# Kernel tuning notes

Hardware: AMD Instinct MI355X
Metric: run time of the kernel (lower is better)

## Reference

```python
import jax, jax.numpy as jnp
import numpy as np

D_MODEL = 1024
N_HEADS = 16


def setup_inputs() -> dict:
    key = jax.random.key(0)
    ks = jax.random.split(key, 5)
    B, T, C = 4, 2048, D_MODEL
    x = jax.random.normal(ks[0], (B, T, C), dtype=jnp.float32)
    W_attn = jax.random.normal(ks[1], (C, 3 * C), dtype=jnp.float32) * (1.0 / np.sqrt(C))
    b_attn = jnp.zeros((3 * C,), dtype=jnp.float32)
    W_proj = jax.random.normal(ks[2], (C, C), dtype=jnp.float32) * (1.0 / np.sqrt(C))
    b_proj = jnp.zeros((C,), dtype=jnp.float32)
    return {"x": x, "W_attn": W_attn, "b_attn": b_attn, "W_proj": W_proj, "b_proj": b_proj}


def reference(x, W_attn, b_attn, W_proj, b_proj):
    B, T, C = x.shape
    H = N_HEADS
    hd = C // H
    qkv = x @ W_attn + b_attn                      # [B,T,3C]
    q, k, v = jnp.split(qkv, 3, axis=2)
    # [B,T,C] -> [B,H,T,hd]
    q = q.reshape(B, T, H, hd).transpose(0, 2, 1, 3)
    k = k.reshape(B, T, H, hd).transpose(0, 2, 1, 3)
    v = v.reshape(B, T, H, hd).transpose(0, 2, 1, 3)
    scale = 1.0 / jnp.sqrt(jnp.float32(hd))
    attn = jnp.einsum('bhqd,bhkd->bhqk', q, k) * scale
    causal = jnp.tril(jnp.ones((T, T), dtype=bool))
    attn = jnp.where(causal[None, None], attn, -jnp.inf)
    w = jax.nn.softmax(attn, axis=-1)
    ctx = jnp.einsum('bhqk,bhkd->bhqd', w, v)      # [B,H,T,hd]
    ctx = ctx.transpose(0, 2, 1, 3).reshape(B, T, C)
    return ctx @ W_proj + b_proj
```

## Files before the change

kernel.cpp:

```cpp
#include <hip/hip_runtime.h>
#include <hip/hip_bf16.h>

typedef __bf16 bf16x8 __attribute__((ext_vector_type(8)));
typedef __bf16 bf16x4 __attribute__((ext_vector_type(4)));
typedef float f32x4 __attribute__((ext_vector_type(4)));

#define MFMA(A, B, C) __builtin_amdgcn_mfma_f32_16x16x32_bf16((A), (B), (C), 0, 0, 0)

#if __has_builtin(__builtin_amdgcn_exp2f)
#define EXP2(x) __builtin_amdgcn_exp2f(x)
#else
#define EXP2(x) exp2f(x)
#endif

#define T_SEQ 2048
#define BATCH 4
#define CDIM  1024
#define HEADS 16
#define HD    64
#define MROWS (BATCH * T_SEQ)
#define QK_SCALE 0.18033688011112042f
#define KTILES (CDIM / 64)

__device__ __forceinline__ void async_ld16(const __bf16* g, __bf16* l) {
    __builtin_amdgcn_global_load_lds(
        (const __attribute__((address_space(1))) void*)g,
        (__attribute__((address_space(3))) void*)l, 16, 0, 0);
}

__global__ __launch_bounds__(256) void conv_transpose(const float* __restrict__ src,
                                                      __bf16* __restrict__ dst,
                                                      int R, int C)
{
    __shared__ float tile[32][33];
    int c0 = blockIdx.x * 32, r0 = blockIdx.y * 32;
    int tx = threadIdx.x, ty = threadIdx.y;
#pragma unroll
    for (int i = 0; i < 4; i++)
        tile[ty + i * 8][tx] = src[(long)(r0 + ty + i * 8) * C + c0 + tx];
    __syncthreads();
#pragma unroll
    for (int i = 0; i < 4; i++)
        dst[(long)(c0 + ty + i * 8) * R + r0 + tx] = (__bf16)tile[tx][ty + i * 8];
}

__global__ __launch_bounds__(256) void conv_bf16(const float* __restrict__ src,
                                                 __bf16* __restrict__ dst)
{
    long i = ((long)blockIdx.x * 256 + threadIdx.x) * 8;
    f32x4 f0 = ((const f32x4*)(src + i))[0];
    f32x4 f1 = ((const f32x4*)(src + i))[1];
    bf16x8 v;
#pragma unroll
    for (int j = 0; j < 4; j++) { v[j] = (__bf16)f0[j]; v[4 + j] = (__bf16)f1[j]; }
    *(bf16x8*)(dst + i) = v;
}

__global__ __launch_bounds__(256) void vtrans(const __bf16* __restrict__ qkv,
                                              __bf16* __restrict__ vt)
{
    __shared__ __bf16 tile[32][33];
    int bh = blockIdx.z;
    int b = bh >> 4, h = bh & 15;
    int t0 = blockIdx.x * 32, d0 = blockIdx.y * 32;
    int tx = threadIdx.x, ty = threadIdx.y;
#pragma unroll
    for (int i = 0; i < 4; i++)
        tile[ty + i * 8][tx] =
            qkv[(long)(b * T_SEQ + t0 + ty + i * 8) * (3 * CDIM) + 2 * CDIM + h * HD + d0 + tx];
    __syncthreads();
#pragma unroll
    for (int i = 0; i < 4; i++)
        vt[(long)(bh * HD + d0 + ty + i * 8) * T_SEQ + t0 + tx] = tile[tx][ty + i * 8];
}

#define STAGE_A(buf, kt, s)                                                      \
    do {                                                                         \
        async_ld16(Asrc + (long)((s) * 64) * lda + (kt) * 64,                    \
                   &lds[buf][0][(s) * 4096 + sdst]);                             \
        async_ld16(Asrc + (long)((s) * 64 + 128) * lda + (kt) * 64,              \
                   &lds[buf][0][(s) * 4096 + 8192 + sdst]);                      \
    } while (0)

#define STAGE_B(buf, kt, s)                                                      \
    do {                                                                         \
        async_ld16(Bsrc + (long)((s) * 128) * CDIM + (kt) * 64,                  \
                   &lds[buf][1][(s) * 8192 + sdst]);                             \
        async_ld16(Bsrc + (long)((s) * 128 + 64) * CDIM + (kt) * 64,             \
                   &lds[buf][1][(s) * 8192 + 4096 + sdst]);                      \
    } while (0)

template <bool OUT_F32>
__global__ __launch_bounds__(512, 2) void gemm8p(const __bf16* __restrict__ A,
                                                 const __bf16* __restrict__ Bt,
                                                 const float* __restrict__ bias,
                                                 void* __restrict__ Cv,
                                                 int N, int lda, int scale_cols)
{
    __shared__ __attribute__((aligned(16))) __bf16 lds[2][2][256 * 64];

    const int nwg = (int)gridDim.x;
    const int bid = (int)blockIdx.x;
    const int swz = (bid & 7) * (nwg >> 3) + (bid >> 3);
    const int nbx = N >> 8;
    const int n0 = (swz % nbx) * 256;
    const int m0 = (swz / nbx) * 256;

    const int t = threadIdx.x;
    const int wave = t >> 6, lane = t & 63;
    const int quad = lane >> 4, l15 = lane & 15;
    const int wm = wave >> 2;
    const int wn = wave & 3;

    const int srow = t >> 3;
    const int scol = ((t & 7) * 8) ^ ((srow & 7) << 3);
    const int sdst = srow * 64 + (t & 7) * 8;
    const __bf16* Asrc = A + (long)(m0 + srow) * lda + scol;
    const __bf16* Bsrc = Bt + (long)(n0 + srow) * CDIM + scol;

    const int kx0 = (quad * 8) ^ ((l15 & 7) << 3);
    const int kx1 = (32 + quad * 8) ^ ((l15 & 7) << 3);
    const int arow = (wm * 128 + l15) * 64;
    const int brow = (wn * 64 + l15) * 64;

    f32x4 acc[8][4] = {};
    bf16x8 a[4][2], bb[4][2];

    STAGE_A(0, 0, 0); STAGE_B(0, 0, 0); STAGE_B(0, 0, 1); STAGE_A(0, 0, 1);
    STAGE_A(1, 1, 0); STAGE_B(1, 1, 0); STAGE_B(1, 1, 1);
    asm volatile("s_waitcnt vmcnt(6)" ::: "memory");
    __builtin_amdgcn_s_barrier();

    for (int kt = 0; kt < KTILES; ++kt) {
        const int cur = kt & 1;
        const __bf16* Ac = &lds[cur][0][0];
        const __bf16* Bc = &lds[cur][1][0];

#pragma unroll
        for (int mf = 0; mf < 4; mf++) {
            a[mf][0] = *(const bf16x8*)&Ac[arow + mf * 1024 + kx0];
            a[mf][1] = *(const bf16x8*)&Ac[arow + mf * 1024 + kx1];
        }
#pragma unroll
        for (int nf = 0; nf < 2; nf++) {
            bb[nf][0] = *(const bf16x8*)&Bc[brow + nf * 1024 + kx0];
            bb[nf][1] = *(const bf16x8*)&Bc[brow + nf * 1024 + kx1];
        }
        if (kt + 1 < KTILES) STAGE_A((kt + 1) & 1, kt + 1, 1);
        __builtin_amdgcn_s_barrier();
        asm volatile("s_waitcnt lgkmcnt(0)" ::: "memory");
        __builtin_amdgcn_s_setprio(1);
#pragma unroll
        for (int mf = 0; mf < 4; mf++)
#pragma unroll
            for (int nf = 0; nf < 2; nf++) {
                acc[mf][nf] = MFMA(a[mf][0], bb[nf][0], acc[mf][nf]);
                acc[mf][nf] = MFMA(a[mf][1], bb[nf][1], acc[mf][nf]);
            }
        __builtin_amdgcn_s_setprio(0);
        __builtin_amdgcn_s_barrier();

#pragma unroll
        for (int nf = 2; nf < 4; nf++) {
            bb[nf][0] = *(const bf16x8*)&Bc[brow + nf * 1024 + kx0];
            bb[nf][1] = *(const bf16x8*)&Bc[brow + nf * 1024 + kx1];
        }
        if (kt + 2 < KTILES) STAGE_A(cur, kt + 2, 0);
        __builtin_amdgcn_s_barrier();
        asm volatile("s_waitcnt lgkmcnt(0)" ::: "memory");
        __builtin_amdgcn_s_setprio(1);
#pragma unroll
        for (int mf = 0; mf < 4; mf++)
#pragma unroll
            for (int nf = 2; nf < 4; nf++) {
                acc[mf][nf] = MFMA(a[mf][0], bb[nf][0], acc[mf][nf]);
                acc[mf][nf] = MFMA(a[mf][1], bb[nf][1], acc[mf][nf]);
            }
        __builtin_amdgcn_s_setprio(0);
        __builtin_amdgcn_s_barrier();

#pragma unroll
        for (int mf = 0; mf < 4; mf++) {
            a[mf][0] = *(const bf16x8*)&Ac[arow + 4096 + mf * 1024 + kx0];
            a[mf][1] = *(const bf16x8*)&Ac[arow + 4096 + mf * 1024 + kx1];
        }
        if (kt + 2 < KTILES) STAGE_B(cur, kt + 2, 0);
        __builtin_amdgcn_s_barrier();
        asm volatile("s_waitcnt lgkmcnt(0)" ::: "memory");
        __builtin_amdgcn_s_setprio(1);
#pragma unroll
        for (int mf = 0; mf < 4; mf++)
#pragma unroll
            for (int nf = 2; nf < 4; nf++) {
                acc[4 + mf][nf] = MFMA(a[mf][0], bb[nf][0], acc[4 + mf][nf]);
                acc[4 + mf][nf] = MFMA(a[mf][1], bb[nf][1], acc[4 + mf][nf]);
            }
        __builtin_amdgcn_s_setprio(0);
        __builtin_amdgcn_s_barrier();

        if (kt + 2 < KTILES) STAGE_B(cur, kt + 2, 1);
        __builtin_amdgcn_s_barrier();
        __builtin_amdgcn_s_setprio(1);
#pragma unroll
        for (int mf = 0; mf < 4; mf++)
#pragma unroll
            for (int nf = 0; nf < 2; nf++) {
                acc[4 + mf][nf] = MFMA(a[mf][0], bb[nf][0], acc[4 + mf][nf]);
                acc[4 + mf][nf] = MFMA(a[mf][1], bb[nf][1], acc[4 + mf][nf]);
            }
        __builtin_amdgcn_s_setprio(0);
        if (kt < KTILES - 2) { asm volatile("s_waitcnt vmcnt(6)" ::: "memory"); }
        else                 { asm volatile("s_waitcnt vmcnt(0)" ::: "memory"); }
        __builtin_amdgcn_s_barrier();
    }

    const float sc = (n0 < scale_cols) ? QK_SCALE : 1.0f;
#pragma unroll
    for (int mf = 0; mf < 8; mf++) {
#pragma unroll
        for (int nf = 0; nf < 4; nf++) {
            const int col = n0 + wn * 64 + nf * 16 + l15;
            const float bv = bias[col];
#pragma unroll
            for (int r = 0; r < 4; r++) {
                const int row = m0 + wm * 128 + mf * 16 + quad * 4 + r;
                float v = (acc[mf][nf][r] + bv) * sc;
                if constexpr (OUT_F32)
                    ((float*)Cv)[(long)row * N + col] = v;
                else
                    ((__bf16*)Cv)[(long)row * N + col] = (__bf16)v;
            }
        }
    }
}

__global__ __launch_bounds__(256) void attn_kernel(__bf16* qkv,
                                                   const __bf16* __restrict__ vt)
{
    __shared__ __attribute__((aligned(16))) __bf16 Ks[2][64 * 32];
    __shared__ __attribute__((aligned(16))) __bf16 Vts[2][64 * 32];
    __shared__ __attribute__((aligned(16))) __bf16 Ps[8][16 * 72];

    const int bh = blockIdx.x;
    const int b = bh >> 4, h = bh & 15;
    const int qt = (int)gridDim.y - 1 - (int)blockIdx.y;
    const int q0 = qt * 128;
    const int t = threadIdx.x;
    const int wave = t >> 6, lane = t & 63;
    const int quad = lane >> 4, l15 = lane & 15;

    bf16x8 qfr[2][2];
#pragma unroll
    for (int f = 0; f < 2; f++) {
        const __bf16* qb = qkv + (long)(b * T_SEQ + q0 + f * 64 + wave * 16 + l15) * (3 * CDIM) + h * HD;
        qfr[f][0] = *(const bf16x8*)(qb + quad * 8);
        qfr[f][1] = *(const bf16x8*)(qb + 32 + quad * 8);
    }

    bf16x8 vone;
#pragma unroll
    for (int j = 0; j < 8; j++) vone[j] = (__bf16)1.0f;

    f32x4 Oacc[2][4] = {};
    f32x4 lacc[2] = {};

    const __bf16* kbase = qkv + (long)(b * T_SEQ + (t >> 2)) * (3 * CDIM)
                          + CDIM + h * HD + (t & 3) * 8;
    const __bf16* vbase = vt + ((long)bh * HD + (t >> 2)) * T_SEQ + (t & 3) * 8;

    const int ntiles = (q0 + 128) / 64;
    for (int kt = 0; kt < ntiles; kt++) {
        const __bf16* kp = kbase + (long)kt * 64 * (3 * CDIM);
        async_ld16(kp,      &Ks[0][t * 8]);
        async_ld16(kp + 32, &Ks[1][t * 8]);
        const __bf16* vp = vbase + kt * 64;
        async_ld16(vp,      &Vts[0][t * 8]);
        async_ld16(vp + 32, &Vts[1][t * 8]);
        __syncthreads();

#pragma unroll
        for (int c = 0; c < 4; c++) {
            bf16x8 kf0 = *(const bf16x8*)&Ks[0][(c * 16 + l15) * 32 + quad * 8];
            bf16x8 kf1 = *(const bf16x8*)&Ks[1][(c * 16 + l15) * 32 + quad * 8];
#pragma unroll
            for (int f = 0; f < 2; f++) {
                f32x4 z = {};
                z = MFMA(kf0, qfr[f][0], z);
                z = MFMA(kf1, qfr[f][1], z);
                const int qbf = q0 + f * 64 + wave * 16;
                const int qg = qbf + l15;
                const int kvb = kt * 64 + c * 16 + quad * 4;
                bf16x4 pk;
                if (kt * 64 + 63 > qbf) {
#pragma unroll
                    for (int r = 0; r < 4; r++) {
                        float v = (kvb + r > qg) ? -1e30f : z[r];
                        pk[r] = (__bf16)EXP2(v);
                    }
                } else {
#pragma unroll
                    for (int r = 0; r < 4; r++)
                        pk[r] = (__bf16)EXP2(z[r]);
                }
                *(bf16x4*)&Ps[wave * 2 + f][l15 * 72 + c * 16 + quad * 4] = pk;
            }
        }

        __threadfence_block();

        bf16x8 pf[2][2];
#pragma unroll
        for (int f = 0; f < 2; f++) {
            pf[f][0] = *(const bf16x8*)&Ps[wave * 2 + f][l15 * 72 + quad * 8];
            pf[f][1] = *(const bf16x8*)&Ps[wave * 2 + f][l15 * 72 + 32 + quad * 8];
            lacc[f] = MFMA(pf[f][0], vone, lacc[f]);
            lacc[f] = MFMA(pf[f][1], vone, lacc[f]);
        }
#pragma unroll
        for (int n = 0; n < 4; n++) {
            bf16x8 vf0 = *(const bf16x8*)&Vts[0][(n * 16 + l15) * 32 + quad * 8];
            bf16x8 vf1 = *(const bf16x8*)&Vts[1][(n * 16 + l15) * 32 + quad * 8];
#pragma unroll
            for (int f = 0; f < 2; f++) {
                Oacc[f][n] = MFMA(pf[f][0], vf0, Oacc[f][n]);
                Oacc[f][n] = MFMA(pf[f][1], vf1, Oacc[f][n]);
            }
        }
        __syncthreads();
    }

#pragma unroll
    for (int f = 0; f < 2; f++)
#pragma unroll
        for (int n = 0; n < 4; n++) {
            int col = h * HD + n * 16 + l15;
#pragma unroll
            for (int r = 0; r < 4; r++) {
                int row = q0 + f * 64 + wave * 16 + quad * 4 + r;
                float val = Oacc[f][n][r] / lacc[f][r];
                qkv[(long)(b * T_SEQ + row) * (3 * CDIM) + col] = (__bf16)val;
            }
        }
}

extern "C" void kernel_launch(void* const* d_in, const int* in_sizes, int n_in,
                              void* d_out, int out_size, void* d_ws, size_t ws_size,
                              hipStream_t stream) {
    (void)in_sizes; (void)n_in; (void)out_size; (void)ws_size;
    const float* x  = (const float*)d_in[0];
    const float* Wa = (const float*)d_in[1];
    const float* ba = (const float*)d_in[2];
    const float* Wp = (const float*)d_in[3];
    const float* bp = (const float*)d_in[4];
    float* out = (float*)d_out;

    char* ws = (char*)d_ws;
    __bf16* qkv = (__bf16*)(ws);
    __bf16* Wat = (__bf16*)(ws + 50331648);
    __bf16* vt  = (__bf16*)(ws + 50331648);
    __bf16* Wpt = (__bf16*)(ws + 50331648);
    __bf16* xbf = (__bf16*)d_out;

    conv_bf16<<<dim3(MROWS * CDIM / (256 * 8)), 256, 0, stream>>>(x, xbf);
    conv_transpose<<<dim3(3 * CDIM / 32, CDIM / 32), dim3(32, 8), 0, stream>>>(Wa, Wat, CDIM, 3 * CDIM);

    gemm8p<false><<<dim3((MROWS / 256) * (3 * CDIM / 256)), 512, 0, stream>>>(
        xbf, Wat, ba, qkv, 3 * CDIM, CDIM, CDIM);

    vtrans<<<dim3(T_SEQ / 32, HD / 32, BATCH * HEADS), dim3(32, 8), 0, stream>>>(qkv, vt);

    attn_kernel<<<dim3(BATCH * HEADS, T_SEQ / 128), 256, 0, stream>>>(qkv, vt);

    conv_transpose<<<dim3(CDIM / 32, CDIM / 32), dim3(32, 8), 0, stream>>>(Wp, Wpt, CDIM, CDIM);

    gemm8p<true><<<dim3((MROWS / 256) * (CDIM / 256)), 512, 0, stream>>>(
        qkv, Wpt, bp, out, CDIM, 3 * CDIM, 0);
}
```

Measured before the change: 262.4 us.

## Split GEMM into specialized QKV and projection kernels with retuned tiles and register prefetch

```diff
diff --git a/kernel.cpp b/kernel.cpp
--- a/kernel.cpp
+++ b/kernel.cpp
@@ -74,161 +74,328 @@
         vt[(long)(bh * HD + d0 + ty + i * 8) * T_SEQ + t0 + tx] = tile[tx][ty + i * 8];
 }
 
-#define STAGE_A(buf, kt, s)                                                      \
+
+#define QS_ALO(p, kt)                                                            \
     do {                                                                         \
-        async_ld16(Asrc + (long)((s) * 64) * lda + (kt) * 64,                    \
-                   &lds[buf][0][(s) * 4096 + sdst]);                             \
-        async_ld16(Asrc + (long)((s) * 64 + 128) * lda + (kt) * 64,              \
-                   &lds[buf][0][(s) * 4096 + 8192 + sdst]);                      \
+        async_ld16(Asrc + (long)(kt) * 64, &Ab[p][sdst]);                        \
+        async_ld16(Asrc + (long)128 * CDIM + (kt) * 64, &Ab[p][8192 + sdst]);    \
     } while (0)
-
-#define STAGE_B(buf, kt, s)                                                      \
+#define QS_AHI(p, kt)                                                            \
     do {                                                                         \
-        async_ld16(Bsrc + (long)((s) * 128) * CDIM + (kt) * 64,                  \
-                   &lds[buf][1][(s) * 8192 + sdst]);                             \
-        async_ld16(Bsrc + (long)((s) * 128 + 64) * CDIM + (kt) * 64,             \
-                   &lds[buf][1][(s) * 8192 + 4096 + sdst]);                      \
+        async_ld16(Asrc + (long)64 * CDIM + (kt) * 64, &Ab[p][4096 + sdst]);     \
+        async_ld16(Asrc + (long)192 * CDIM + (kt) * 64, &Ab[p][12288 + sdst]);   \
     } while (0)
-
-template <bool OUT_F32>
-__global__ __launch_bounds__(512, 2) void gemm8p(const __bf16* __restrict__ A,
-                                                 const __bf16* __restrict__ Bt,
-                                                 const float* __restrict__ bias,
-                                                 void* __restrict__ Cv,
-                                                 int N, int lda, int scale_cols)
+#define QS_B(p, kt)                                                              \
+    do {                                                                         \
+        async_ld16(Bsrc + (long)(kt) * 64, &Bb[p][sdst]);                        \
+        async_ld16(Bsrc + (long)64 * CDIM + (kt) * 64, &Bb[p][4096 + sdst]);     \
+        async_ld16(Bsrc + (long)128 * CDIM + (kt) * 64, &Bb[p][8192 + sdst]);    \
+    } while (0)
+
+__global__ __launch_bounds__(512, 2) void gemm_qkv(const __bf16* __restrict__ A,
+                                                   const __bf16* __restrict__ Bt,
+                                                   const float* __restrict__ bias,
+                                                   __bf16* __restrict__ C)
 {
-    __shared__ __attribute__((aligned(16))) __bf16 lds[2][2][256 * 64];
-
-    const int nwg = (int)gridDim.x;
+    __shared__ __attribute__((aligned(16))) __bf16 Ab[2][256 * 64];
+    __shared__ __attribute__((aligned(16))) __bf16 Bb[2][192 * 64];
+
     const int bid = (int)blockIdx.x;
-    const int swz = (bid & 7) * (nwg >> 3) + (bid >> 3);
-    const int nbx = N >> 8;
-    const int n0 = (swz % nbx) * 256;
-    const int m0 = (swz / nbx) * 256;
+    const int swz = (bid & 7) * 64 + (bid >> 3);
+    const int n0 = (swz & 15) * 192;
+    const int m0 = (swz >> 4) * 256;
 
     const int t = threadIdx.x;
     const int wave = t >> 6, lane = t & 63;
     const int quad = lane >> 4, l15 = lane & 15;
-    const int wm = wave >> 2;
-    const int wn = wave & 3;
+    const int wm = wave >> 2, wn = wave & 3;
 
     const int srow = t >> 3;
     const int scol = ((t & 7) * 8) ^ ((srow & 7) << 3);
     const int sdst = srow * 64 + (t & 7) * 8;
-    const __bf16* Asrc = A + (long)(m0 + srow) * lda + scol;
+    const __bf16* Asrc = A + (long)(m0 + srow) * CDIM + scol;
     const __bf16* Bsrc = Bt + (long)(n0 + srow) * CDIM + scol;
 
     const int kx0 = (quad * 8) ^ ((l15 & 7) << 3);
     const int kx1 = (32 + quad * 8) ^ ((l15 & 7) << 3);
-    const int arow = (wm * 128 + l15) * 64;
-    const int brow = (wn * 64 + l15) * 64;
-
-    f32x4 acc[8][4] = {};
-    bf16x8 a[4][2], bb[4][2];
-
-    STAGE_A(0, 0, 0); STAGE_B(0, 0, 0); STAGE_B(0, 0, 1); STAGE_A(0, 0, 1);
-    STAGE_A(1, 1, 0); STAGE_B(1, 1, 0); STAGE_B(1, 1, 1);
+    const int aro = (wm * 128 + l15) * 64;
+    const int bro = (wn * 48 + l15) * 64;
+
+    f32x4 acc[8][3] = {};
+    bf16x8 A0[4][2], A1[4][2], B0[2][2], B1[2];
+
+    QS_ALO(0, 0); QS_AHI(0, 0); QS_B(0, 0);
+    QS_ALO(1, 1); QS_AHI(1, 1); QS_B(1, 1);
+    asm volatile("s_waitcnt vmcnt(7)" ::: "memory");
+    __builtin_amdgcn_s_barrier();
+#pragma unroll
+    for (int mf = 0; mf < 4; mf++) {
+        A0[mf][0] = *(const bf16x8*)&Ab[0][aro + mf * 1024 + kx0];
+        A0[mf][1] = *(const bf16x8*)&Ab[0][aro + mf * 1024 + kx1];
+    }
+#pragma unroll
+    for (int nf = 0; nf < 2; nf++) {
+        B0[nf][0] = *(const bf16x8*)&Bb[0][bro + nf * 1024 + kx0];
+        B0[nf][1] = *(const bf16x8*)&Bb[0][bro + nf * 1024 + kx1];
+    }
+
+#pragma unroll 2
+    for (int kt = 0; kt < KTILES; ++kt) {
+        const int cur = kt & 1, nxt = cur ^ 1;
+
+#pragma unroll
+        for (int mf = 0; mf < 4; mf++) {
+            A1[mf][0] = *(const bf16x8*)&Ab[cur][aro + 4096 + mf * 1024 + kx0];
+            A1[mf][1] = *(const bf16x8*)&Ab[cur][aro + 4096 + mf * 1024 + kx1];
+        }
+        __builtin_amdgcn_s_barrier();
+        asm volatile("s_waitcnt lgkmcnt(8)");
+        __builtin_amdgcn_sched_barrier(0);
+        __builtin_amdgcn_s_setprio(1);
+#pragma unroll
+        for (int mf = 0; mf < 4; mf++)
+#pragma unroll
+            for (int nf = 0; nf < 2; nf++) {
+                acc[mf][nf] = MFMA(A0[mf][0], B0[nf][0], acc[mf][nf]);
+                acc[mf][nf] = MFMA(A0[mf][1], B0[nf][1], acc[mf][nf]);
+            }
+        __builtin_amdgcn_s_setprio(0);
+        __builtin_amdgcn_s_barrier();
+
+        B1[0] = *(const bf16x8*)&Bb[cur][bro + 2048 + kx0];
+        B1[1] = *(const bf16x8*)&Bb[cur][bro + 2048 + kx1];
+        if (kt + 2 < KTILES) QS_ALO(cur, kt + 2);
+        __builtin_amdgcn_s_barrier();
+        asm volatile("s_waitcnt lgkmcnt(2)");
+        __builtin_amdgcn_sched_barrier(0);
+        __builtin_amdgcn_s_setprio(1);
+#pragma unroll
+        for (int mf = 0; mf < 4; mf++)
+#pragma unroll
+            for (int nf = 0; nf < 2; nf++) {
+                acc[4 + mf][nf] = MFMA(A1[mf][0], B0[nf][0], acc[4 + mf][nf]);
+                acc[4 + mf][nf] = MFMA(A1[mf][1], B0[nf][1], acc[4 + mf][nf]);
+            }
+        __builtin_amdgcn_s_setprio(0);
+        if (kt + 2 < KTILES) { asm volatile("s_waitcnt vmcnt(2)" ::: "memory"); }
+        else                 { asm volatile("s_waitcnt vmcnt(0)" ::: "memory"); }
+        __builtin_amdgcn_s_barrier();
+
+        if (kt + 2 < KTILES) QS_AHI(cur, kt + 2);
+        if (kt + 1 < KTILES) {
+#pragma unroll
+            for (int nf = 0; nf < 2; nf++) {
+                B0[nf][0] = *(const bf16x8*)&Bb[nxt][bro + nf * 1024 + kx0];
+                B0[nf][1] = *(const bf16x8*)&Bb[nxt][bro + nf * 1024 + kx1];
+            }
+        }
+        __builtin_amdgcn_s_barrier();
+        asm volatile("s_waitcnt lgkmcnt(4)");
+        __builtin_amdgcn_sched_barrier(0);
+        __builtin_amdgcn_s_setprio(1);
+#pragma unroll
+        for (int mf = 0; mf < 4; mf++) {
+            acc[mf][2] = MFMA(A0[mf][0], B1[0], acc[mf][2]);
+            acc[mf][2] = MFMA(A0[mf][1], B1[1], acc[mf][2]);
+        }
+        __builtin_amdgcn_s_setprio(0);
+        __builtin_amdgcn_s_barrier();
+
+        if (kt + 2 < KTILES) QS_B(cur, kt + 2);
+        if (kt + 1 < KTILES) {
+#pragma unroll
+            for (int mf = 0; mf < 4; mf++) {
+                A0[mf][0] = *(const bf16x8*)&Ab[nxt][aro + mf * 1024 + kx0];
+                A0[mf][1] = *(const bf16x8*)&Ab[nxt][aro + mf * 1024 + kx1];
+            }
+        }
+        __builtin_amdgcn_s_barrier();
+        asm volatile("s_waitcnt lgkmcnt(8)");
+        __builtin_amdgcn_sched_barrier(0);
+        __builtin_amdgcn_s_setprio(1);
+#pragma unroll
+        for (int mf = 0; mf < 4; mf++) {
+            acc[4 + mf][2] = MFMA(A1[mf][0], B1[0], acc[4 + mf][2]);
+            acc[4 + mf][2] = MFMA(A1[mf][1], B1[1], acc[4 + mf][2]);
+        }
+        __builtin_amdgcn_s_setprio(0);
+        __builtin_amdgcn_s_barrier();
+    }
+
+#pragma unroll
+    for (int mf = 0; mf < 8; mf++) {
+#pragma unroll
+        for (int nf = 0; nf < 3; nf++) {
+            const int col = n0 + wn * 48 + nf * 16 + l15;
+            const float bv = bias[col];
+            const float sc = (col < CDIM) ? QK_SCALE : 1.0f;
+#pragma unroll
+            for (int r = 0; r < 4; r++) {
+                const int row = m0 + wm * 128 + (mf >> 2) * 64 + (mf & 3) * 16 + quad * 4 + r;
+                C[(long)row * (3 * CDIM) + col] = (__bf16)((acc[mf][nf][r] + bv) * sc);
+            }
+        }
+    }
+}
+
+#define PS_A(p, kt)                                                              \
+    do {                                                                         \
+        async_ld16(Asrc + (long)(kt) * 64, &Ab[p][sdst]);                        \
+        async_ld16(Asrc + (long)64 * (3 * CDIM) + (kt) * 64, &Ab[p][4096 + sdst]); \
+    } while (0)
+#define PS_B(p, kt)                                                              \
+    do {                                                                         \
+        async_ld16(Bsrc + (long)(kt) * 64, &Bb[p][sdst]);                        \
+        async_ld16(Bsrc + (long)64 * CDIM + (kt) * 64, &Bb[p][4096 + sdst]);     \
+        async_ld16(Bsrc + (long)128 * CDIM + (kt) * 64, &Bb[p][8192 + sdst]);    \
+        async_ld16(Bsrc + (long)192 * CDIM + (kt) * 64, &Bb[p][12288 + sdst]);   \
+    } while (0)
+
+__global__ __launch_bounds__(512, 2) void gemm_proj(const __bf16* __restrict__ A,
+                                                    const __bf16* __restrict__ Bt,
+                                                    const float* __restrict__ bias,
+                                                    float* __restrict__ C)
+{
+    __shared__ __attribute__((aligned(16))) __bf16 Ab[2][128 * 64];
+    __shared__ __attribute__((aligned(16))) __bf16 Bb[2][256 * 64];
+
+    const int bid = (int)blockIdx.x;
+    const int swz = (bid & 7) * 32 + (bid >> 3);
+    const int n0 = (swz & 3) * 256;
+    const int m0 = (swz >> 2) * 128;
+
+    const int t = threadIdx.x;
+    const int wave = t >> 6, lane = t & 63;
+    const int quad = lane >> 4, l15 = lane & 15;
+    const int wm = wave >> 2, wn = wave & 3;
+
+    const int srow = t >> 3;
+    const int scol = ((t & 7) * 8) ^ ((srow & 7) << 3);
+    const int sdst = srow * 64 + (t & 7) * 8;
+    const __bf16* Asrc = A + (long)(m0 + srow) * (3 * CDIM) + scol;
+    const __bf16* Bsrc = Bt + (long)(n0 + srow) * CDIM + scol;
+
+    const int kx0 = (quad * 8) ^ ((l15 & 7) << 3);
+    const int kx1 = (32 + quad * 8) ^ ((l15 & 7) << 3);
+    const int aro = (wm * 64 + l15) * 64;
+    const int bro = (wn * 64 + l15) * 64;
+
+    f32x4 acc[4][4] = {};
+    bf16x8 A0[2][2], A1[2][2], B0[2][2], B1[2][2];
+
+    PS_A(0, 0); PS_B(0, 0);
+    PS_A(1, 1); PS_B(1, 1);
     asm volatile("s_waitcnt vmcnt(6)" ::: "memory");
     __builtin_amdgcn_s_barrier();
-
+#pragma unroll
+    for (int mf = 0; mf < 2; mf++) {
+        A0[mf][0] = *(const bf16x8*)&Ab[0][aro + mf * 1024 + kx0];
+        A0[mf][1] = *(const bf16x8*)&Ab[0][aro + mf * 1024 + kx1];
+    }
+#pragma unroll
+    for (int nf = 0; nf < 2; nf++) {
+        B0[nf][0] = *(const bf16x8*)&Bb[0][bro + nf * 1024 + kx0];
+        B0[nf][1] = *(const bf16x8*)&Bb[0][bro + nf * 1024 + kx1];
+    }
+
+#pragma unroll 2
     for (int kt = 0; kt < KTILES; ++kt) {
-        const int cur = kt & 1;
-        const __bf16* Ac = &lds[cur][0][0];
-        const __bf16* Bc = &lds[cur][1][0];
-
-#pragma unroll
-        for (int mf = 0; mf < 4; mf++) {
-            a[mf][0] = *(const bf16x8*)&Ac[arow + mf * 1024 + kx0];
-            a[mf][1] = *(const bf16x8*)&Ac[arow + mf * 1024 + kx1];
-        }
+        const int cur = kt & 1, nxt = cur ^ 1;
+
+#pragma unroll
+        for (int mf = 0; mf < 2; mf++) {
+            A1[mf][0] = *(const bf16x8*)&Ab[cur][aro + 2048 + mf * 1024 + kx0];
+            A1[mf][1] = *(const bf16x8*)&Ab[cur][aro + 2048 + mf * 1024 + kx1];
+        }
+        __builtin_amdgcn_s_barrier();
+        asm volatile("s_waitcnt lgkmcnt(4)");
+        __builtin_amdgcn_sched_barrier(0);
+        __builtin_amdgcn_s_setprio(1);
+#pragma unroll
+        for (int mf = 0; mf < 2; mf++)
+#pragma unroll
+            for (int nf = 0; nf < 2; nf++) {
+                acc[mf][nf] = MFMA(A0[mf][0], B0[nf][0], acc[mf][nf]);
+                acc[mf][nf] = MFMA(A0[mf][1], B0[nf][1], acc[mf][nf]);
+            }
+        __builtin_amdgcn_s_setprio(0);
+        __builtin_amdgcn_s_barrier();
+
 #pragma unroll
         for (int nf = 0; nf < 2; nf++) {
-            bb[nf][0] = *(const bf16x8*)&Bc[brow + nf * 1024 + kx0];
-            bb[nf][1] = *(const bf16x8*)&Bc[brow + nf * 1024 + kx1];
-        }
-        if (kt + 1 < KTILES) STAGE_A((kt + 1) & 1, kt + 1, 1);
-        __builtin_amdgcn_s_barrier();
-        asm volatile("s_waitcnt lgkmcnt(0)" ::: "memory");
-        __builtin_amdgcn_s_setprio(1);
-#pragma unroll
-        for (int mf = 0; mf < 4; mf++)
-#pragma unroll
-            for (int nf = 0; nf < 2; nf++) {
-                acc[mf][nf] = MFMA(a[mf][0], bb[nf][0], acc[mf][nf]);
-                acc[mf][nf] = MFMA(a[mf][1], bb[nf][1], acc[mf][nf]);
-            }
-        __builtin_amdgcn_s_setprio(0);
-        __builtin_amdgcn_s_barrier();
-
-#pragma unroll
-        for (int nf = 2; nf < 4; nf++) {
-            bb[nf][0] = *(const bf16x8*)&Bc[brow + nf * 1024 + kx0];
-            bb[nf][1] = *(const bf16x8*)&Bc[brow + nf * 1024 + kx1];
-        }
-        if (kt + 2 < KTILES) STAGE_A(cur, kt + 2, 0);
-        __builtin_amdgcn_s_barrier();
-        asm volatile("s_waitcnt lgkmcnt(0)" ::: "memory");
-        __builtin_amdgcn_s_setprio(1);
-#pragma unroll
-        for (int mf = 0; mf < 4; mf++)
-#pragma unroll
-            for (int nf = 2; nf < 4; nf++) {
-                acc[mf][nf] = MFMA(a[mf][0], bb[nf][0], acc[mf][nf]);
-                acc[mf][nf] = MFMA(a[mf][1], bb[nf][1], acc[mf][nf]);
-            }
-        __builtin_amdgcn_s_setprio(0);
-        __builtin_amdgcn_s_barrier();
-
-#pragma unroll
-        for (int mf = 0; mf < 4; mf++) {
-            a[mf][0] = *(const bf16x8*)&Ac[arow + 4096 + mf * 1024 + kx0];
-            a[mf][1] = *(const bf16x8*)&Ac[arow + 4096 + mf * 1024 + kx1];
-        }
-        if (kt + 2 < KTILES) STAGE_B(cur, kt + 2, 0);
-        __builtin_amdgcn_s_barrier();
-        asm volatile("s_waitcnt lgkmcnt(0)" ::: "memory");
-        __builtin_amdgcn_s_setprio(1);
-#pragma unroll
-        for (int mf = 0; mf < 4; mf++)
-#pragma unroll
-            for (int nf = 2; nf < 4; nf++) {
-                acc[4 + mf][nf] = MFMA(a[mf][0], bb[nf][0], acc[4 + mf][nf]);
-                acc[4 + mf][nf] = MFMA(a[mf][1], bb[nf][1], acc[4 + mf][nf]);
-            }
-        __builtin_amdgcn_s_setprio(0);
-        __builtin_amdgcn_s_barrier();
-
-        if (kt + 2 < KTILES) STAGE_B(cur, kt + 2, 1);
-        __builtin_amdgcn_s_barrier();
-        __builtin_amdgcn_s_setprio(1);
-#pragma unroll
-        for (int mf = 0; mf < 4; mf++)
-#pragma unroll
-            for (int nf = 0; nf < 2; nf++) {
-                acc[4 + mf][nf] = MFMA(a[mf][0], bb[nf][0], acc[4 + mf][nf]);
-                acc[4 + mf][nf] = MFMA(a[mf][1], bb[nf][1], acc[4 + mf][nf]);
-            }
-        __builtin_amdgcn_s_setprio(0);
-        if (kt < KTILES - 2) { asm volatile("s_waitcnt vmcnt(6)" ::: "memory"); }
-        else                 { asm volatile("s_waitcnt vmcnt(0)" ::: "memory"); }
-        __builtin_amdgcn_s_barrier();
-    }
-
-    const float sc = (n0 < scale_cols) ? QK_SCALE : 1.0f;
-#pragma unroll
-    for (int mf = 0; mf < 8; mf++) {
+            B1[nf][0] = *(const bf16x8*)&Bb[cur][bro + 2048 + nf * 1024 + kx0];
+            B1[nf][1] = *(const bf16x8*)&Bb[cur][bro + 2048 + nf * 1024 + kx1];
+        }
+        __builtin_amdgcn_s_barrier();
+        asm volatile("s_waitcnt lgkmcnt(4)");
+        __builtin_amdgcn_sched_barrier(0);
+        __builtin_amdgcn_s_setprio(1);
+#pragma unroll
+        for (int mf = 0; mf < 2; mf++)
+#pragma unroll
+            for (int nf = 0; nf < 2; nf++) {
+                acc[2 + mf][nf] = MFMA(A1[mf][0], B0[nf][0], acc[2 + mf][nf]);
+                acc[2 + mf][nf] = MFMA(A1[mf][1], B0[nf][1], acc[2 + mf][nf]);
+            }
+        __builtin_amdgcn_s_setprio(0);
+        asm volatile("s_waitcnt vmcnt(0)" ::: "memory");
+        __builtin_amdgcn_s_barrier();
+
+        if (kt + 2 < KTILES) PS_A(cur, kt + 2);
+        if (kt + 1 < KTILES) {
+#pragma unroll
+            for (int nf = 0; nf < 2; nf++) {
+                B0[nf][0] = *(const bf16x8*)&Bb[nxt][bro + nf * 1024 + kx0];
+                B0[nf][1] = *(const bf16x8*)&Bb[nxt][bro + nf * 1024 + kx1];
+            }
+        }
+        __builtin_amdgcn_s_barrier();
+        asm volatile("s_waitcnt lgkmcnt(4)");
+        __builtin_amdgcn_sched_barrier(0);
+        __builtin_amdgcn_s_setprio(1);
+#pragma unroll
+        for (int mf = 0; mf < 2; mf++)
+#pragma unroll
+            for (int nf = 0; nf < 2; nf++) {
+                acc[mf][2 + nf] = MFMA(A0[mf][0], B1[nf][0], acc[mf][2 + nf]);
+                acc[mf][2 + nf] = MFMA(A0[mf][1], B1[nf][1], acc[mf][2 + nf]);
+            }
+        __builtin_amdgcn_s_setprio(0);
+        __builtin_amdgcn_s_barrier();
+
+        if (kt + 2 < KTILES) PS_B(cur, kt + 2);
+        if (kt + 1 < KTILES) {
+#pragma unroll
+            for (int mf = 0; mf < 2; mf++) {
+                A0[mf][0] = *(const bf16x8*)&Ab[nxt][aro + mf * 1024 + kx0];
+                A0[mf][1] = *(const bf16x8*)&Ab[nxt][aro + mf * 1024 + kx1];
+            }
+        }
+        __builtin_amdgcn_s_barrier();
+        asm volatile("s_waitcnt lgkmcnt(4)");
+        __builtin_amdgcn_sched_barrier(0);
+        __builtin_amdgcn_s_setprio(1);
+#pragma unroll
+        for (int mf = 0; mf < 2; mf++)
+#pragma unroll
+            for (int nf = 0; nf < 2; nf++) {
+                acc[2 + mf][2 + nf] = MFMA(A1[mf][0], B1[nf][0], acc[2 + mf][2 + nf]);
+                acc[2 + mf][2 + nf] = MFMA(A1[mf][1], B1[nf][1], acc[2 + mf][2 + nf]);
+            }
+        __builtin_amdgcn_s_setprio(0);
+        __builtin_amdgcn_s_barrier();
+    }
+
+#pragma unroll
+    for (int mf = 0; mf < 4; mf++) {
 #pragma unroll
         for (int nf = 0; nf < 4; nf++) {
-            const int col = n0 + wn * 64 + nf * 16 + l15;
+            const int col = n0 + wn * 64 + (nf >> 1) * 32 + (nf & 1) * 16 + l15;
             const float bv = bias[col];
 #pragma unroll
             for (int r = 0; r < 4; r++) {
-                const int row = m0 + wm * 128 + mf * 16 + quad * 4 + r;
-                float v = (acc[mf][nf][r] + bv) * sc;
-                if constexpr (OUT_F32)
-                    ((float*)Cv)[(long)row * N + col] = v;
-                else
-                    ((__bf16*)Cv)[(long)row * N + col] = (__bf16)v;
+                const int row = m0 + wm * 64 + (mf >> 1) * 32 + (mf & 1) * 16 + quad * 4 + r;
+                C[(long)row * CDIM + col] = acc[mf][nf][r] + bv;
             }
         }
     }
@@ -364,8 +531,7 @@
     conv_bf16<<<dim3(MROWS * CDIM / (256 * 8)), 256, 0, stream>>>(x, xbf);
     conv_transpose<<<dim3(3 * CDIM / 32, CDIM / 32), dim3(32, 8), 0, stream>>>(Wa, Wat, CDIM, 3 * CDIM);
 
-    gemm8p<false><<<dim3((MROWS / 256) * (3 * CDIM / 256)), 512, 0, stream>>>(
-        xbf, Wat, ba, qkv, 3 * CDIM, CDIM, CDIM);
+    gemm_qkv<<<dim3(512), 512, 0, stream>>>(xbf, Wat, ba, qkv);
 
     vtrans<<<dim3(T_SEQ / 32, HD / 32, BATCH * HEADS), dim3(32, 8), 0, stream>>>(qkv, vt);
 
@@ -373,6 +539,5 @@
 
     conv_transpose<<<dim3(CDIM / 32, CDIM / 32), dim3(32, 8), 0, stream>>>(Wp, Wpt, CDIM, CDIM);
 
-    gemm8p<true><<<dim3((MROWS / 256) * (CDIM / 256)), 512, 0, stream>>>(
-        qkv, Wpt, bp, out, CDIM, 3 * CDIM, 0);
-}
+    gemm_proj<<<dim3(256), 512, 0, stream>>>(qkv, Wpt, bp, out);
+}
```

After: 258.2 us. About the same (-1.6%).
